# Optimization experiments

Hardware: AMD Instinct MI355X
Metric: run time of the kernel (lower is better)

Reference implementation:

```python
import jax, jax.numpy as jnp
import numpy as np

B, L, H, T, C = 4, 256, 768, 16, 6
SIM_THR = 0.0
EPS_LN = 1e-5


def layer_norm(x, g, b):
    m = x.mean(-1, keepdims=True)
    v = ((x - m) ** 2).mean(-1, keepdims=True)
    return (x - m) / jnp.sqrt(v + EPS_LN) * g + b


def setup_inputs() -> dict:
    key = jax.random.key(0)
    ks = jax.random.split(key, 20)
    s = 0.02
    embeddings = jax.random.normal(ks[0], (B, L, H), jnp.float32)
    masks = jnp.ones((B, L, L), jnp.float32)
    asp_st = jax.random.randint(ks[1], (B, T), 0, 12)
    asp_ed = asp_st + jax.random.randint(ks[2], (B, T), 0, 3)
    opi_st = jax.random.randint(ks[3], (B, T), 0, 12)
    opi_ed = opi_st + jax.random.randint(ks[4], (B, T), 0, 3)
    sent_id = jax.random.randint(ks[5], (B, T), 2, 5)
    return {
        "embeddings": embeddings, "masks": masks,
        "asp_st": asp_st, "asp_ed": asp_ed, "opi_st": opi_st, "opi_ed": opi_ed,
        "sent_id": sent_id,
        "edge_embed": jax.random.normal(ks[6], (2, H), jnp.float32) * s,
        "W_tp": jax.random.normal(ks[7], (2 * H + 3, H), jnp.float32) * s,
        "b_tp": jnp.zeros((H,), jnp.float32),
        "W_attn": jax.random.normal(ks[8], (3 * H, 1), jnp.float32) * s,
        "b_attn": jnp.zeros((1,), jnp.float32),
        "W_gat": jax.random.normal(ks[9], (2 * H, H), jnp.float32) * s,
        "b_gat": jnp.zeros((H,), jnp.float32),
        "gamma0": jnp.ones((H,), jnp.float32), "beta0": jnp.zeros((H,), jnp.float32),
        "W1": jax.random.normal(ks[10], (2 * H, L), jnp.float32) * s,
        "bl1": jnp.zeros((L,), jnp.float32),
        "gamma1": jnp.ones((L,), jnp.float32), "beta1": jnp.zeros((L,), jnp.float32),
        "Wc": jax.random.normal(ks[11], (L, C), jnp.float32) * s,
        "bc": jnp.zeros((C,), jnp.float32),
        "Wc1": jax.random.normal(ks[12], (L, 2), jnp.float32) * s,
        "bc1": jnp.zeros((2,), jnp.float32),
    }


def _triplet_enhance(emb_b, a_st, a_ed, o_st, o_ed, sid,
                     edge_embed, W_tp, b_tp, W_attn, b_attn, W_gat, b_gat):
    # emb_b: [L,H]; span ints: [T]
    pos = jnp.arange(L)
    am = (pos[None, :] >= a_st[:, None]) & (pos[None, :] <= a_ed[:, None])  # [T,L]
    om = (pos[None, :] >= o_st[:, None]) & (pos[None, :] <= o_ed[:, None])
    amf = am.astype(emb_b.dtype)
    omf = om.astype(emb_b.dtype)
    asp = (amf @ emb_b) / amf.sum(1, keepdims=True)  # [T,H] span-mean
    opi = (omf @ emb_b) / omf.sum(1, keepdims=True)
    sv = jax.nn.one_hot(sid - 2, 3, dtype=emb_b.dtype)  # [T,3]
    nf = jnp.concatenate([asp, opi, sv], -1) @ W_tp + b_tp  # [T,H]

    # cosine similarity between triplet nodes
    nrm = nf / jnp.maximum(jnp.linalg.norm(nf, axis=-1, keepdims=True), 1e-8)
    sim = nrm @ nrm.T
    eye = jnp.eye(T, dtype=bool)
    ok = (sim > SIM_THR) & ~eye
    m0 = ok & (a_st[:, None] == a_st[None, :]) & (a_ed[:, None] == a_ed[None, :])
    m1 = ok & (o_st[:, None] == o_st[None, :]) & (o_ed[:, None] == o_ed[None, :])
    # edge (i,j): src=i, tgt=j -> incoming mask indexed [tgt, src, etype]
    emask = jnp.stack([m0.T, m1.T], axis=-1)  # [T,T,2]

    E = edge_embed  # [2,H]
    cc = jnp.concatenate([
        jnp.broadcast_to(nf[:, None, None, :], (T, T, 2, H)),   # target feats
        jnp.broadcast_to(nf[None, :, None, :], (T, T, 2, H)),   # source feats
        jnp.broadcast_to(E[None, None, :, :], (T, T, 2, H)),
    ], -1)  # [T,T,2,3H]
    scores = (jax.nn.leaky_relu(cc, 0.2) @ W_attn)[..., 0] + b_attn[0]  # [T,T,2]
    neg = jnp.where(emask, scores, -1e9)
    attn = jax.nn.softmax(neg.reshape(T, -1), axis=-1).reshape(T, T, 2)
    msg = jnp.concatenate([
        jnp.broadcast_to(nf[:, None, :], (T, 2, H)),
        jnp.broadcast_to(E[None, :, :], (T, 2, H)),
    ], -1)  # [src, etype, 2H]
    agg = jnp.einsum('tse,sef->tf', attn, msg)
    upd = jax.nn.relu(agg @ W_gat + b_gat)
    has_in = emask.any(axis=(1, 2))
    new_nf = jnp.where(has_in[:, None], upd, nf)
    has_edges = emask.any().astype(emb_b.dtype)  # original skips scatter if no edges
    center = (a_st + o_st) // 2
    return emb_b.at[center].add(new_nf * has_edges)


def reference(embeddings, masks, asp_st, asp_ed, opi_st, opi_ed, sent_id,
              edge_embed, W_tp, b_tp, W_attn, b_attn, W_gat, b_gat,
              gamma0, beta0, W1, bl1, gamma1, beta1, Wc, bc, Wc1, bc1):
    emb1 = layer_norm(embeddings, gamma0, beta0)
    emb = jax.vmap(_triplet_enhance,
                   in_axes=(0, 0, 0, 0, 0, 0) + (None,) * 7)(
        emb1, asp_st, asp_ed, opi_st, opi_ed, sent_id,
        edge_embed, W_tp, b_tp, W_attn, b_attn, W_gat, b_gat)

    # cat([feat_exp, feat_expT]) @ W1  ==  emb@W1[:H] (rows) + emb@W1[H:] (cols)
    A = jnp.einsum('bih,hk->bik', emb, W1[:H])
    Bm = jnp.einsum('bjh,hk->bjk', emb, W1[H:])
    hidden = A[:, :, None, :] + Bm[:, None, :, :] + bl1  # [B,L,L,L]
    hidden = jax.nn.gelu(layer_norm(hidden, gamma1, beta1), approximate=False)
    logits = (hidden @ Wc + bc) * masks[..., None]    # [B,L,L,C]
    logits1 = (hidden @ Wc1 + bc1) * masks[..., None]  # [B,L,L,2]
    return jnp.concatenate([logits, logits1], -1)
```

## Files before the change

kernel.cpp:

```cpp
#include <hip/hip_runtime.h>

__device__ __forceinline__ unsigned short f2bf(float f) {
    union { float f; unsigned u; } v; v.f = f;
    unsigned u = v.u;
    unsigned r = (u + 0x7fffu + ((u >> 16) & 1u)) >> 16;
    return (unsigned short)r;
}
__device__ __forceinline__ float bfup(int x) {
    union { unsigned u; float f; } v; v.u = ((unsigned)(unsigned short)x) << 16; return v.f;
}

typedef __attribute__((ext_vector_type(8))) short short8;
typedef __attribute__((ext_vector_type(4))) float floatx4;

#define Bn 4
#define Ln 256
#define Hn 768
#define Tn 16

__global__ __launch_bounds__(256) void k_ln0(const float* __restrict__ x,
                                             const float* __restrict__ g,
                                             const float* __restrict__ be,
                                             float* __restrict__ out) {
    int row = blockIdx.x, tid = threadIdx.x;
    const float* xr = x + (size_t)row * Hn;
    float v0 = xr[tid], v1 = xr[tid + 256], v2 = xr[tid + 512];
    float s = v0 + v1 + v2;
    float q = v0 * v0 + v1 * v1 + v2 * v2;
    __shared__ float sm[4], qm[4];
    for (int o = 32; o > 0; o >>= 1) { s += __shfl_down(s, o); q += __shfl_down(q, o); }
    if ((tid & 63) == 0) { sm[tid >> 6] = s; qm[tid >> 6] = q; }
    __syncthreads();
    float S = sm[0] + sm[1] + sm[2] + sm[3];
    float Q = qm[0] + qm[1] + qm[2] + qm[3];
    float mean = S * (1.f / 768.f);
    float rstd = rsqrtf(Q * (1.f / 768.f) - mean * mean + 1e-5f);
    float* o0 = out + (size_t)row * Hn;
    o0[tid]       = (v0 - mean) * rstd * g[tid]       + be[tid];
    o0[tid + 256] = (v1 - mean) * rstd * g[tid + 256] + be[tid + 256];
    o0[tid + 512] = (v2 - mean) * rstd * g[tid + 512] + be[tid + 512];
}

__global__ __launch_bounds__(256) void k_spans(const float* __restrict__ emb,
                                               const int* __restrict__ ast_, const int* __restrict__ aed_,
                                               const int* __restrict__ ost_, const int* __restrict__ oed_,
                                               const int* __restrict__ sid_,
                                               float* __restrict__ xv,
                                               float* __restrict__ nf) {
    int n = blockIdx.x, b = n >> 4, tid = threadIdx.x;
    int ast = ast_[n], aed = aed_[n], ost = ost_[n], oed = oed_[n], sid = sid_[n];
    float ai = 1.f / (float)(aed - ast + 1);
    float oi = 1.f / (float)(oed - ost + 1);
    const float* eb = emb + (size_t)b * Ln * Hn;
    float* xr = xv + (size_t)n * 1568;
    for (int r = tid; r < 1568; r += 256) {
        float v;
        if (r < 768) {
            float s = 0.f;
            for (int l = ast; l <= aed; ++l) s += eb[l * Hn + r];
            v = s * ai;
        } else if (r < 1536) {
            int h = r - 768;
            float s = 0.f;
            for (int l = ost; l <= oed; ++l) s += eb[l * Hn + h];
            v = s * oi;
        } else if (r < 1539) {
            v = (sid - 2 == r - 1536) ? 1.f : 0.f;
        } else {
            v = 0.f;
        }
        xr[r] = v;
    }
    float* nr = nf + (size_t)n * Hn;
    nr[tid] = 0.f; nr[tid + 256] = 0.f; nr[tid + 512] = 0.f;
}

__global__ __launch_bounds__(256) void k_skinny(const float* __restrict__ A,
                                                const float* __restrict__ B,
                                                const float* __restrict__ bias,
                                                float* __restrict__ C,
                                                int Kpad, int Kb, int Kc) {
    __shared__ float At[32][33], Bt[32][33];
    int tid = threadIdx.x;
    int n0 = blockIdx.x * 32, m0 = blockIdx.y * 32, z = blockIdx.z;
    int kbeg = z * Kc;
    int kend = kbeg + Kc; if (kend > Kpad) kend = Kpad;
    int lr = tid >> 3, lc = (tid & 7) * 4;
    int tm = tid >> 3, tn4 = (tid & 7) * 4;
    float acc0 = 0.f, acc1 = 0.f, acc2 = 0.f, acc3 = 0.f;
    for (int k0 = kbeg; k0 < kend; k0 += 32) {
        float4 av = *(const float4*)(A + (size_t)(m0 + lr) * Kpad + k0 + lc);
        At[lr][lc] = av.x; At[lr][lc + 1] = av.y; At[lr][lc + 2] = av.z; At[lr][lc + 3] = av.w;
        int gk = k0 + lr;
        float4 bv = {0.f, 0.f, 0.f, 0.f};
        if (gk < Kb) bv = *(const float4*)(B + (size_t)gk * 768 + n0 + lc);
        Bt[lr][lc] = bv.x; Bt[lr][lc + 1] = bv.y; Bt[lr][lc + 2] = bv.z; Bt[lr][lc + 3] = bv.w;
        __syncthreads();
#pragma unroll
        for (int k = 0; k < 32; ++k) {
            float a = At[tm][k];
            acc0 = fmaf(a, Bt[k][tn4], acc0);
            acc1 = fmaf(a, Bt[k][tn4 + 1], acc1);
            acc2 = fmaf(a, Bt[k][tn4 + 2], acc2);
            acc3 = fmaf(a, Bt[k][tn4 + 3], acc3);
        }
        __syncthreads();
    }
    if (z == 0) {
        acc0 += bias[n0 + tn4];
        acc1 += bias[n0 + tn4 + 1];
        acc2 += bias[n0 + tn4 + 2];
        acc3 += bias[n0 + tn4 + 3];
    }
    float* dst = C + (size_t)(m0 + tm) * 768 + n0 + tn4;
    atomicAdd(&dst[0], acc0);
    atomicAdd(&dst[1], acc1);
    atomicAdd(&dst[2], acc2);
    atomicAdd(&dst[3], acc3);
}

__global__ __launch_bounds__(256) void k_graph(const float* __restrict__ nf,
                                               const int* __restrict__ ast_, const int* __restrict__ aed_,
                                               const int* __restrict__ ost_, const int* __restrict__ oed_,
                                               const float* __restrict__ E,
                                               const float* __restrict__ Wat,
                                               const float* __restrict__ bat,
                                               int* __restrict__ hasin, float* __restrict__ hasedge,
                                               float* __restrict__ agg, float* __restrict__ raw) {
    int b = blockIdx.x, tid = threadIdx.x;
    __shared__ float nfs[16][780];
    __shared__ float Es[2][768];
    __shared__ int ast[16], aed[16], ost[16], oed[16];
    __shared__ float red[256];
    __shared__ float nrm[16], p[16], q[16], rr[2];
    __shared__ float ws2[16][16];
    __shared__ float aes[16][2];
    __shared__ unsigned m0b[16], m1b[16];
    const float* nfb = nf + (size_t)b * 16 * Hn;
    for (int e = tid; e < 3072; e += 256) {
        int r = e / 192, c = (e - r * 192) * 4;
        float4 v = *(const float4*)(nfb + r * Hn + c);
        nfs[r][c] = v.x; nfs[r][c + 1] = v.y; nfs[r][c + 2] = v.z; nfs[r][c + 3] = v.w;
    }
    for (int e = tid; e < 1536; e += 256) ((float*)Es)[e] = E[e];
    if (tid < 16) {
        int n = b * 16 + tid;
        ast[tid] = ast_[n]; aed[tid] = aed_[n]; ost[tid] = ost_[n]; oed[tid] = oed_[n];
        m0b[tid] = 0u; m1b[tid] = 0u;
    }
    __syncthreads();
    int t = tid >> 4, lane = tid & 15;
    float ss = 0.f, pp = 0.f, qq = 0.f;
    for (int h = lane; h < 768; h += 16) {
        float v = nfs[t][h];
        ss = fmaf(v, v, ss);
        float lr = v > 0.f ? v : 0.2f * v;
        pp = fmaf(lr, Wat[h], pp);
        qq = fmaf(lr, Wat[768 + h], qq);
    }
    red[tid] = ss; __syncthreads();
    if (tid < 16) { float s = 0.f; for (int k2 = 0; k2 < 16; ++k2) s += red[tid * 16 + k2]; nrm[tid] = sqrtf(s); }
    __syncthreads();
    red[tid] = pp; __syncthreads();
    if (tid < 16) { float s = 0.f; for (int k2 = 0; k2 < 16; ++k2) s += red[tid * 16 + k2]; p[tid] = s; }
    __syncthreads();
    red[tid] = qq; __syncthreads();
    if (tid < 16) { float s = 0.f; for (int k2 = 0; k2 < 16; ++k2) s += red[tid * 16 + k2]; q[tid] = s; }
    __syncthreads();
    float rp = 0.f;
    if (tid < 32) {
        int e = tid >> 4;
        for (int h = lane; h < 768; h += 16) {
            float v = Es[e][h];
            float lr = v > 0.f ? v : 0.2f * v;
            rp = fmaf(lr, Wat[1536 + h], rp);
        }
    }
    red[tid] = rp; __syncthreads();
    if (tid < 2) { float s = 0.f; for (int k2 = 0; k2 < 16; ++k2) s += red[tid * 16 + k2]; rr[tid] = s; }
    __syncthreads();
    {
        int i = tid >> 4, j = tid & 15;
        const float4* ri = (const float4*)nfs[i];
        const float4* rj = (const float4*)nfs[j];
        float dot = 0.f;
#pragma unroll 4
        for (int h4 = 0; h4 < 192; ++h4) {
            float4 a = ri[h4], c = rj[h4];
            dot = fmaf(a.x, c.x, dot); dot = fmaf(a.y, c.y, dot);
            dot = fmaf(a.z, c.z, dot); dot = fmaf(a.w, c.w, dot);
        }
        float sim = dot / (fmaxf(nrm[i], 1e-8f) * fmaxf(nrm[j], 1e-8f));
        bool ok = (sim > 0.f) && (i != j);
        if (ok && ast[i] == ast[j] && aed[i] == aed[j]) atomicOr(&m0b[i], 1u << j);
        if (ok && ost[i] == ost[j] && oed[i] == oed[j]) atomicOr(&m1b[i], 1u << j);
    }
    __syncthreads();
    if (tid < 16) {
        int tt = tid;
        float battn = bat[0];
        float sc[32];
        float mx = -3.4e38f;
        bool hi = false;
#pragma unroll
        for (int s = 0; s < 16; ++s) {
            bool e0 = (m0b[s] >> tt) & 1u;
            bool e1 = (m1b[s] >> tt) & 1u;
            float base = p[tt] + q[s] + battn;
            float v0 = e0 ? (base + rr[0]) : -1e9f;
            float v1 = e1 ? (base + rr[1]) : -1e9f;
            sc[2 * s] = v0; sc[2 * s + 1] = v1;
            mx = fmaxf(mx, fmaxf(v0, v1));
            hi = hi || e0 || e1;
        }
        float sum = 0.f;
#pragma unroll
        for (int k2 = 0; k2 < 32; ++k2) { float e = expf(sc[k2] - mx); sc[k2] = e; sum += e; }
        float inv = 1.f / sum;
        float ae0 = 0.f, ae1 = 0.f;
#pragma unroll
        for (int s = 0; s < 16; ++s) {
            float w0 = sc[2 * s] * inv, w1 = sc[2 * s + 1] * inv;
            ws2[tt][s] = w0 + w1;
            ae0 += w0; ae1 += w1;
        }
        aes[tt][0] = ae0; aes[tt][1] = ae1;
        hasin[b * 16 + tt] = hi ? 1 : 0;
        red[tid] = hi ? 1.f : 0.f;
    }
    __syncthreads();
    if (tid == 0) {
        float he = 0.f;
        for (int k2 = 0; k2 < 16; ++k2) he = fmaxf(he, red[k2]);
        hasedge[b] = he;
    }
    for (int nn = 0; nn < 16; ++nn) {
        int n = b * 16 + nn;
        float ae0 = aes[nn][0], ae1 = aes[nn][1];
        float* ag = agg + (size_t)n * 1536;
        float* rw = raw + (size_t)n * Hn;
        for (int f = tid; f < 768; f += 256) {
            float s = 0.f;
#pragma unroll
            for (int s16 = 0; s16 < 16; ++s16) s = fmaf(ws2[nn][s16], nfs[s16][f], s);
            ag[f] = s;
            ag[768 + f] = ae0 * Es[0][f] + ae1 * Es[1][f];
            rw[f] = 0.f;
        }
    }
}

__global__ __launch_bounds__(256) void k_scatter(const float* __restrict__ raw,
                                                 const float* __restrict__ nf,
                                                 const int* __restrict__ hasin, const float* __restrict__ hasedge,
                                                 const int* __restrict__ ast_, const int* __restrict__ ost_,
                                                 float* __restrict__ emb) {
    int n = blockIdx.x, b = n >> 4, tid = threadIdx.x;
    if (hasedge[b] == 0.f) return;
    int center = (ast_[n] + ost_[n]) >> 1;
    float* dst = emb + (size_t)(b * Ln + center) * Hn;
    int hi = hasin[n];
    const float* src = hi ? (raw + (size_t)n * Hn) : (nf + (size_t)n * Hn);
    for (int h = tid; h < 768; h += 256) {
        float v = src[h];
        if (hi) v = fmaxf(v, 0.f);
        atomicAdd(&dst[h], v);
    }
}

__global__ __launch_bounds__(256) void k_w1t(const float* __restrict__ W1,
                                             unsigned short* __restrict__ w1t) {
    __shared__ float tile[32][33];
    int kt = blockIdx.x, nt = blockIdx.y, tid = threadIdx.x;
    int k0 = kt * 32, n0 = nt * 32;
    int rowoff = (n0 < 256) ? 0 : 768;
    int col0 = n0 & 255;
    int r = tid >> 3, c = (tid & 7) * 4;
    float4 v = *(const float4*)(W1 + (size_t)(rowoff + k0 + r) * 256 + col0 + c);
    tile[r][c] = v.x; tile[r][c + 1] = v.y; tile[r][c + 2] = v.z; tile[r][c + 3] = v.w;
    __syncthreads();
    ushort4 o;
    o.x = f2bf(tile[c][r]); o.y = f2bf(tile[c + 1][r]);
    o.z = f2bf(tile[c + 2][r]); o.w = f2bf(tile[c + 3][r]);
    *(ushort4*)(w1t + (size_t)(n0 + r) * 768 + k0 + c) = o;
}

__global__ __launch_bounds__(64) void k_gemm(const float* __restrict__ emb,
                                             const unsigned short* __restrict__ w1t,
                                             float* __restrict__ abm) {
    int wid = blockIdx.x;
    int m0 = (wid >> 4) * 32;
    int n0 = (wid & 15) * 32;
    int lane = threadIdx.x;
    int r = lane & 15, g = lane >> 4;
    const float* Af0 = emb + (size_t)(m0 + r) * 768 + g * 8;
    const float* Af1 = emb + (size_t)(m0 + 16 + r) * 768 + g * 8;
    const short8* Bp0 = (const short8*)(w1t + (size_t)(n0 + r) * 768 + g * 8);
    const short8* Bp1 = (const short8*)(w1t + (size_t)(n0 + 16 + r) * 768 + g * 8);
    floatx4 acc00 = {0.f, 0.f, 0.f, 0.f}, acc01 = {0.f, 0.f, 0.f, 0.f};
    floatx4 acc10 = {0.f, 0.f, 0.f, 0.f}, acc11 = {0.f, 0.f, 0.f, 0.f};
#pragma unroll 4
    for (int ks = 0; ks < 768; ks += 32) {
        float4 x0 = *(const float4*)(Af0 + ks);
        float4 x1 = *(const float4*)(Af0 + ks + 4);
        float4 y0 = *(const float4*)(Af1 + ks);
        float4 y1 = *(const float4*)(Af1 + ks + 4);
        short8 a0, a1;
        union { float f; unsigned u; } cv;
#define PK(dst, idx, val) { cv.f = (val); dst[idx] = (short)((cv.u + 0x8000u) >> 16); }
        PK(a0, 0, x0.x) PK(a0, 1, x0.y) PK(a0, 2, x0.z) PK(a0, 3, x0.w)
        PK(a0, 4, x1.x) PK(a0, 5, x1.y) PK(a0, 6, x1.z) PK(a0, 7, x1.w)
        PK(a1, 0, y0.x) PK(a1, 1, y0.y) PK(a1, 2, y0.z) PK(a1, 3, y0.w)
        PK(a1, 4, y1.x) PK(a1, 5, y1.y) PK(a1, 6, y1.z) PK(a1, 7, y1.w)
#undef PK
        short8 b0 = Bp0[ks >> 3];
        short8 b1 = Bp1[ks >> 3];
        acc00 = __builtin_amdgcn_mfma_f32_16x16x32_bf16(a0, b0, acc00, 0, 0, 0);
        acc01 = __builtin_amdgcn_mfma_f32_16x16x32_bf16(a0, b1, acc01, 0, 0, 0);
        acc10 = __builtin_amdgcn_mfma_f32_16x16x32_bf16(a1, b0, acc10, 0, 0, 0);
        acc11 = __builtin_amdgcn_mfma_f32_16x16x32_bf16(a1, b1, acc11, 0, 0, 0);
    }
#pragma unroll
    for (int t = 0; t < 4; ++t) {
        int row = g * 4 + t;
        abm[(size_t)(m0 + row) * 512 + n0 + r]           = acc00[t];
        abm[(size_t)(m0 + row) * 512 + n0 + 16 + r]      = acc01[t];
        abm[(size_t)(m0 + 16 + row) * 512 + n0 + r]      = acc10[t];
        abm[(size_t)(m0 + 16 + row) * 512 + n0 + 16 + r] = acc11[t];
    }
}

__global__ __launch_bounds__(256) void k_prep(const float* __restrict__ abm,
                                              const float* __restrict__ bl1,
                                              unsigned short* __restrict__ Abf,
                                              unsigned short* __restrict__ Bbf,
                                              float* __restrict__ sA, float* __restrict__ qA,
                                              float* __restrict__ sB, float* __restrict__ qB) {
    int rw = blockIdx.x, tid = threadIdx.x;
    float a = abm[(size_t)rw * 512 + tid];
    float bp = abm[(size_t)rw * 512 + 256 + tid] + bl1[tid];
    Abf[(size_t)rw * 256 + tid] = f2bf(a);
    Bbf[(size_t)rw * 256 + tid] = f2bf(bp);
    float v0 = a, v1 = a * a, v2 = bp, v3 = bp * bp;
    __shared__ float red[4][4];
    for (int o = 32; o > 0; o >>= 1) {
        v0 += __shfl_down(v0, o); v1 += __shfl_down(v1, o);
        v2 += __shfl_down(v2, o); v3 += __shfl_down(v3, o);
    }
    if ((tid & 63) == 0) {
        int w = tid >> 6;
        red[w][0] = v0; red[w][1] = v1; red[w][2] = v2; red[w][3] = v3;
    }
    __syncthreads();
    if (tid == 0) {
        sA[rw] = red[0][0] + red[1][0] + red[2][0] + red[3][0];
        qA[rw] = red[0][1] + red[1][1] + red[2][1] + red[3][1];
        sB[rw] = red[0][2] + red[1][2] + red[2][2] + red[3][2];
        qB[rw] = red[0][3] + red[1][3] + red[2][3] + red[3][3];
    }
}

__global__ __launch_bounds__(256) void k_dots(const float* __restrict__ abm,
                                              const float* __restrict__ bl1,
                                              float* __restrict__ D) {
    __shared__ float At[32][33], Bt[32][33];
    int tid = threadIdx.x;
    int j0 = blockIdx.x * 32, i0 = blockIdx.y * 32, b = blockIdx.z;
    int lr = tid >> 3, lc = (tid & 7) * 4;
    int ti = tid >> 3, tj4 = (tid & 7) * 4;
    float acc0 = 0.f, acc1 = 0.f, acc2 = 0.f, acc3 = 0.f;
    for (int k0 = 0; k0 < 256; k0 += 32) {
        float4 av = *(const float4*)(abm + (size_t)(b * 256 + i0 + lr) * 512 + k0 + lc);
        At[lr][lc] = av.x; At[lr][lc + 1] = av.y; At[lr][lc + 2] = av.z; At[lr][lc + 3] = av.w;
        float4 bv = *(const float4*)(abm + (size_t)(b * 256 + j0 + lr) * 512 + 256 + k0 + lc);
        float4 lv = *(const float4*)(bl1 + k0 + lc);
        Bt[lr][lc] = bv.x + lv.x; Bt[lr][lc + 1] = bv.y + lv.y;
        Bt[lr][lc + 2] = bv.z + lv.z; Bt[lr][lc + 3] = bv.w + lv.w;
        __syncthreads();
#pragma unroll
        for (int k = 0; k < 32; ++k) {
            float a = At[ti][k];
            acc0 = fmaf(a, Bt[tj4][k], acc0);
            acc1 = fmaf(a, Bt[tj4 + 1][k], acc1);
            acc2 = fmaf(a, Bt[tj4 + 2][k], acc2);
            acc3 = fmaf(a, Bt[tj4 + 3][k], acc3);
        }
        __syncthreads();
    }
    float* dst = D + ((size_t)b * 256 + i0 + ti) * 256 + j0 + tj4;
    dst[0] = acc0; dst[1] = acc1; dst[2] = acc2; dst[3] = acc3;
}

__global__ __launch_bounds__(256) void k_hidden2(const unsigned short* __restrict__ Abf,
                                                 const unsigned short* __restrict__ Bbf,
                                                 const float* __restrict__ sA, const float* __restrict__ qA,
                                                 const float* __restrict__ sB, const float* __restrict__ qB,
                                                 const float* __restrict__ D,
                                                 const float* __restrict__ masks,
                                                 const float* __restrict__ g1, const float* __restrict__ b1,
                                                 const float* __restrict__ Wc, const float* __restrict__ bc,
                                                 const float* __restrict__ Wc1, const float* __restrict__ bc1,
                                                 float* __restrict__ out) {
    __shared__ unsigned short As[16][272];
    __shared__ unsigned short Bs[16][272];
    __shared__ unsigned short gsh[256], bsh[256];
    __shared__ short8 Wf[8][64];
    __shared__ float Ds[16][16];
    __shared__ float ms[16][16];
    __shared__ float sAs[16], qAs[16], sBs[16], qBs[16];
    int tid = threadIdx.x;
    int jt = blockIdx.x, it = blockIdx.y, b = blockIdx.z;
    int rowA = b * 256 + it * 16;
    int rowB = b * 256 + jt * 16;
#pragma unroll
    for (int u = 0; u < 2; ++u) {
        int e = tid + u * 256;
        int r = e >> 5, ch = e & 31;
        *(short8*)&As[r][ch * 8] = *(const short8*)(Abf + (size_t)(rowA + r) * 256 + ch * 8);
        *(short8*)&Bs[r][ch * 8] = *(const short8*)(Bbf + (size_t)(rowB + r) * 256 + ch * 8);
    }
    gsh[tid] = f2bf(g1[tid]);
    bsh[tid] = f2bf(b1[tid]);
#pragma unroll
    for (int u = 0; u < 2; ++u) {
        int e = tid + u * 256;
        int s = e >> 6, l = e & 63;
        int qq2 = l >> 4, nn2 = l & 15;
        short8 wv;
#pragma unroll
        for (int t = 0; t < 8; ++t) {
            int k = s * 32 + qq2 * 8 + t;
            float v = (nn2 < 6) ? Wc[k * 6 + nn2] : ((nn2 < 8) ? Wc1[k * 2 + (nn2 - 6)] : 0.f);
            wv[t] = (short)f2bf(v);
        }
        Wf[s][l] = wv;
    }
    {
        int di = tid >> 4, dj = tid & 15;
        size_t gi = ((size_t)(b * 256 + it * 16 + di)) * 256 + jt * 16 + dj;
        Ds[di][dj] = D[gi];
        ms[di][dj] = masks[gi];
    }
    if (tid < 16) {
        sAs[tid] = sA[rowA + tid]; qAs[tid] = qA[rowA + tid];
        sBs[tid] = sB[rowB + tid]; qBs[tid] = qB[rowB + tid];
    }
    __syncthreads();

    int lane = tid & 63, w = tid >> 6;
    int m = lane & 15, q = lane >> 4;
    int iA = w * 4 + (m & 3);
    int n = m;
    float bcs_l = (n < 6) ? bc[n] : ((n < 8) ? bc1[n - 6] : 0.f);
    const float inv256 = 1.f / 256.f;
    const float K1 = -1.5957691216f, K2 = -0.0713548163f;

    for (int p = 0; p < 4; ++p) {
        int jB = p * 4 + (m >> 2);
        float mu = (sAs[iA] + sBs[jB]) * inv256;
        float E2 = (qAs[iA] + 2.f * Ds[iA][jB] + qBs[jB]) * inv256;
        float r_ = rsqrtf(E2 - mu * mu + 1e-5f);
        float c_ = -mu * r_;
        floatx4 acc = {0.f, 0.f, 0.f, 0.f};
#pragma unroll
        for (int s = 0; s < 8; ++s) {
            int ko = s * 32 + q * 8;
            short8 a8 = *(const short8*)&As[iA][ko];
            short8 b8 = *(const short8*)&Bs[jB][ko];
            short8 g8 = *(const short8*)&gsh[ko];
            short8 v8 = *(const short8*)&bsh[ko];
            short8 yv;
#pragma unroll
            for (int t = 0; t < 8; ++t) {
                float h = bfup(a8[t]) + bfup(b8[t]);
                float x = fmaf(h, r_, c_);
                x = fmaf(x, bfup(g8[t]), bfup(v8[t]));
                float mm = fmaf(x * x, K2, K1);
                float e = __expf(x * mm);
                float y = x * __builtin_amdgcn_rcpf(1.f + e);
                union { float f; unsigned u; } cv; cv.f = y;
                yv[t] = (short)((cv.u + 0x8000u) >> 16);
            }
            acc = __builtin_amdgcn_mfma_f32_16x16x32_bf16(yv, Wf[s][lane], acc, 0, 0, 0);
        }
        if (n < 8) {
#pragma unroll
            for (int rg = 0; rg < 4; ++rg) {
                int mp = q * 4 + rg;
                int il = w * 4 + (mp & 3);
                int jl = p * 4 + (mp >> 2);
                float mk = ms[il][jl];
                size_t idx = (((size_t)(b * 256 + it * 16 + il)) * 256 + jt * 16 + jl) * 8 + n;
                out[idx] = (acc[rg] + bcs_l) * mk;
            }
        }
    }
}

extern "C" void kernel_launch(void* const* d_in, const int* in_sizes, int n_in,
                              void* d_out, int out_size, void* d_ws, size_t ws_size,
                              hipStream_t stream) {
    (void)in_sizes; (void)n_in; (void)out_size; (void)ws_size;
    const float* emb_in = (const float*)d_in[0];
    const float* masks  = (const float*)d_in[1];
    const int* ast = (const int*)d_in[2];
    const int* aed = (const int*)d_in[3];
    const int* ost = (const int*)d_in[4];
    const int* oed = (const int*)d_in[5];
    const int* sid = (const int*)d_in[6];
    const float* E    = (const float*)d_in[7];
    const float* Wtp  = (const float*)d_in[8];
    const float* btp  = (const float*)d_in[9];
    const float* Wat  = (const float*)d_in[10];
    const float* bat  = (const float*)d_in[11];
    const float* Wg   = (const float*)d_in[12];
    const float* bg   = (const float*)d_in[13];
    const float* g0   = (const float*)d_in[14];
    const float* b0   = (const float*)d_in[15];
    const float* W1   = (const float*)d_in[16];
    const float* bl1  = (const float*)d_in[17];
    const float* g1   = (const float*)d_in[18];
    const float* b1   = (const float*)d_in[19];
    const float* Wc   = (const float*)d_in[20];
    const float* bc   = (const float*)d_in[21];
    const float* Wc1  = (const float*)d_in[22];
    const float* bc1  = (const float*)d_in[23];
    float* outp = (float*)d_out;

    float* fw = (float*)d_ws;
    float* emb = fw;
    float* nf  = fw + 786432;
    int*   hasin = (int*)(fw + 835584);
    float* hasedge = fw + 835648;
    float* xv  = fw + 835712;
    float* agg = fw + 936064;
    float* raw = fw + 1034368;
    float* Dd  = fw + 835712;
    float* abm = fw + 1097856;
    float* sA  = fw + 1622144;
    float* qA  = fw + 1623168;
    float* sB  = fw + 1624192;
    float* qB  = fw + 1625216;
    unsigned short* Abf = (unsigned short*)(fw + 1626240);
    unsigned short* Bbf = (unsigned short*)(fw + 1757312);
    unsigned short* w1t = (unsigned short*)(fw + 1888384);

    dim3 gw(24, 16);
    k_w1t<<<gw, 256, 0, stream>>>(W1, w1t);
    k_ln0<<<1024, 256, 0, stream>>>(emb_in, g0, b0, emb);
    k_spans<<<64, 256, 0, stream>>>(emb, ast, aed, ost, oed, sid, xv, nf);
    dim3 gs1(24, 2, 7);
    k_skinny<<<gs1, 256, 0, stream>>>(xv, Wtp, btp, nf, 1568, 1539, 224);
    k_graph<<<4, 256, 0, stream>>>(nf, ast, aed, ost, oed, E, Wat, bat, hasin, hasedge, agg, raw);
    k_skinny<<<gs1, 256, 0, stream>>>(agg, Wg, bg, raw, 1536, 1536, 224);
    k_scatter<<<64, 256, 0, stream>>>(raw, nf, hasin, hasedge, ast, ost, emb);
    k_gemm<<<512, 64, 0, stream>>>(emb, w1t, abm);
    k_prep<<<1024, 256, 0, stream>>>(abm, bl1, Abf, Bbf, sA, qA, sB, qB);
    dim3 gd(8, 8, 4);
    k_dots<<<gd, 256, 0, stream>>>(abm, bl1, Dd);
    dim3 g6(16, 16, 4);
    k_hidden2<<<g6, 256, 0, stream>>>(Abf, Bbf, sA, qA, sB, qB, Dd, masks,
                                      g1, b1, Wc, bc, Wc1, bc1, outp);
}
```

Measured before the change: 265.7 us.

## Fuse bf16 prep, row stats and A·B dot products into hidden kernel

Removes the k_prep and k_dots kernels. The hidden kernel now converts the fp32 A/B rows to bf16 itself, computes per-row sums and sums of squares, and computes the 16x16 cross-dot tile with one wave using MFMA. LN0 and the W1 transpose are merged into a single launch, and the LDS pitch is changed. This cuts launches and intermediate global round trips, at the cost of redundant per-tile conversion and reductions. The dot products and stats are now computed from bf16-rounded values, which slightly changes numerics.

```diff
diff --git a/kernel.cpp b/kernel.cpp
--- a/kernel.cpp
+++ b/kernel.cpp
@@ -17,28 +17,49 @@
 #define Ln 256
 #define Hn 768
 #define Tn 16
-
-__global__ __launch_bounds__(256) void k_ln0(const float* __restrict__ x,
+#define PITCH 288
+
+__global__ __launch_bounds__(256) void k_pre(const float* __restrict__ x,
                                              const float* __restrict__ g,
                                              const float* __restrict__ be,
-                                             float* __restrict__ out) {
-    int row = blockIdx.x, tid = threadIdx.x;
-    const float* xr = x + (size_t)row * Hn;
-    float v0 = xr[tid], v1 = xr[tid + 256], v2 = xr[tid + 512];
-    float s = v0 + v1 + v2;
-    float q = v0 * v0 + v1 * v1 + v2 * v2;
-    __shared__ float sm[4], qm[4];
-    for (int o = 32; o > 0; o >>= 1) { s += __shfl_down(s, o); q += __shfl_down(q, o); }
-    if ((tid & 63) == 0) { sm[tid >> 6] = s; qm[tid >> 6] = q; }
-    __syncthreads();
-    float S = sm[0] + sm[1] + sm[2] + sm[3];
-    float Q = qm[0] + qm[1] + qm[2] + qm[3];
-    float mean = S * (1.f / 768.f);
-    float rstd = rsqrtf(Q * (1.f / 768.f) - mean * mean + 1e-5f);
-    float* o0 = out + (size_t)row * Hn;
-    o0[tid]       = (v0 - mean) * rstd * g[tid]       + be[tid];
-    o0[tid + 256] = (v1 - mean) * rstd * g[tid + 256] + be[tid + 256];
-    o0[tid + 512] = (v2 - mean) * rstd * g[tid + 512] + be[tid + 512];
+                                             float* __restrict__ out,
+                                             const float* __restrict__ W1,
+                                             unsigned short* __restrict__ w1t) {
+    int bid = blockIdx.x, tid = threadIdx.x;
+    if (bid < 1024) {
+        int row = bid;
+        const float* xr = x + (size_t)row * Hn;
+        float v0 = xr[tid], v1 = xr[tid + 256], v2 = xr[tid + 512];
+        float s = v0 + v1 + v2;
+        float q = v0 * v0 + v1 * v1 + v2 * v2;
+        __shared__ float sm[4], qm[4];
+        for (int o = 32; o > 0; o >>= 1) { s += __shfl_down(s, o); q += __shfl_down(q, o); }
+        if ((tid & 63) == 0) { sm[tid >> 6] = s; qm[tid >> 6] = q; }
+        __syncthreads();
+        float S = sm[0] + sm[1] + sm[2] + sm[3];
+        float Q = qm[0] + qm[1] + qm[2] + qm[3];
+        float mean = S * (1.f / 768.f);
+        float rstd = rsqrtf(Q * (1.f / 768.f) - mean * mean + 1e-5f);
+        float* o0 = out + (size_t)row * Hn;
+        o0[tid]       = (v0 - mean) * rstd * g[tid]       + be[tid];
+        o0[tid + 256] = (v1 - mean) * rstd * g[tid + 256] + be[tid + 256];
+        o0[tid + 512] = (v2 - mean) * rstd * g[tid + 512] + be[tid + 512];
+    } else {
+        __shared__ float tile[32][33];
+        int idx = bid - 1024;
+        int kt = idx % 24, nt = idx / 24;
+        int k0 = kt * 32, n0 = nt * 32;
+        int rowoff = (n0 < 256) ? 0 : 768;
+        int col0 = n0 & 255;
+        int r = tid >> 3, c = (tid & 7) * 4;
+        float4 v = *(const float4*)(W1 + (size_t)(rowoff + k0 + r) * 256 + col0 + c);
+        tile[r][c] = v.x; tile[r][c + 1] = v.y; tile[r][c + 2] = v.z; tile[r][c + 3] = v.w;
+        __syncthreads();
+        ushort4 o;
+        o.x = f2bf(tile[c][r]); o.y = f2bf(tile[c + 1][r]);
+        o.z = f2bf(tile[c + 2][r]); o.w = f2bf(tile[c + 3][r]);
+        *(ushort4*)(w1t + (size_t)(n0 + r) * 768 + k0 + c) = o;
+    }
 }
 
 __global__ __launch_bounds__(256) void k_spans(const float* __restrict__ emb,
@@ -266,23 +287,6 @@
         if (hi) v = fmaxf(v, 0.f);
         atomicAdd(&dst[h], v);
     }
-}
-
-__global__ __launch_bounds__(256) void k_w1t(const float* __restrict__ W1,
-                                             unsigned short* __restrict__ w1t) {
-    __shared__ float tile[32][33];
-    int kt = blockIdx.x, nt = blockIdx.y, tid = threadIdx.x;
-    int k0 = kt * 32, n0 = nt * 32;
-    int rowoff = (n0 < 256) ? 0 : 768;
-    int col0 = n0 & 255;
-    int r = tid >> 3, c = (tid & 7) * 4;
-    float4 v = *(const float4*)(W1 + (size_t)(rowoff + k0 + r) * 256 + col0 + c);
-    tile[r][c] = v.x; tile[r][c + 1] = v.y; tile[r][c + 2] = v.z; tile[r][c + 3] = v.w;
-    __syncthreads();
-    ushort4 o;
-    o.x = f2bf(tile[c][r]); o.y = f2bf(tile[c + 1][r]);
-    o.z = f2bf(tile[c + 2][r]); o.w = f2bf(tile[c + 3][r]);
-    *(ushort4*)(w1t + (size_t)(n0 + r) * 768 + k0 + c) = o;
 }
 
 __global__ __launch_bounds__(64) void k_gemm(const float* __restrict__ emb,
@@ -330,94 +334,56 @@
     }
 }
 
-__global__ __launch_bounds__(256) void k_prep(const float* __restrict__ abm,
-                                              const float* __restrict__ bl1,
-                                              unsigned short* __restrict__ Abf,
-                                              unsigned short* __restrict__ Bbf,
-                                              float* __restrict__ sA, float* __restrict__ qA,
-                                              float* __restrict__ sB, float* __restrict__ qB) {
-    int rw = blockIdx.x, tid = threadIdx.x;
-    float a = abm[(size_t)rw * 512 + tid];
-    float bp = abm[(size_t)rw * 512 + 256 + tid] + bl1[tid];
-    Abf[(size_t)rw * 256 + tid] = f2bf(a);
-    Bbf[(size_t)rw * 256 + tid] = f2bf(bp);
-    float v0 = a, v1 = a * a, v2 = bp, v3 = bp * bp;
-    __shared__ float red[4][4];
-    for (int o = 32; o > 0; o >>= 1) {
-        v0 += __shfl_down(v0, o); v1 += __shfl_down(v1, o);
-        v2 += __shfl_down(v2, o); v3 += __shfl_down(v3, o);
-    }
-    if ((tid & 63) == 0) {
-        int w = tid >> 6;
-        red[w][0] = v0; red[w][1] = v1; red[w][2] = v2; red[w][3] = v3;
-    }
-    __syncthreads();
-    if (tid == 0) {
-        sA[rw] = red[0][0] + red[1][0] + red[2][0] + red[3][0];
-        qA[rw] = red[0][1] + red[1][1] + red[2][1] + red[3][1];
-        sB[rw] = red[0][2] + red[1][2] + red[2][2] + red[3][2];
-        qB[rw] = red[0][3] + red[1][3] + red[2][3] + red[3][3];
-    }
-}
-
-__global__ __launch_bounds__(256) void k_dots(const float* __restrict__ abm,
-                                              const float* __restrict__ bl1,
-                                              float* __restrict__ D) {
-    __shared__ float At[32][33], Bt[32][33];
-    int tid = threadIdx.x;
-    int j0 = blockIdx.x * 32, i0 = blockIdx.y * 32, b = blockIdx.z;
-    int lr = tid >> 3, lc = (tid & 7) * 4;
-    int ti = tid >> 3, tj4 = (tid & 7) * 4;
-    float acc0 = 0.f, acc1 = 0.f, acc2 = 0.f, acc3 = 0.f;
-    for (int k0 = 0; k0 < 256; k0 += 32) {
-        float4 av = *(const float4*)(abm + (size_t)(b * 256 + i0 + lr) * 512 + k0 + lc);
-        At[lr][lc] = av.x; At[lr][lc + 1] = av.y; At[lr][lc + 2] = av.z; At[lr][lc + 3] = av.w;
-        float4 bv = *(const float4*)(abm + (size_t)(b * 256 + j0 + lr) * 512 + 256 + k0 + lc);
-        float4 lv = *(const float4*)(bl1 + k0 + lc);
-        Bt[lr][lc] = bv.x + lv.x; Bt[lr][lc + 1] = bv.y + lv.y;
-        Bt[lr][lc + 2] = bv.z + lv.z; Bt[lr][lc + 3] = bv.w + lv.w;
-        __syncthreads();
-#pragma unroll
-        for (int k = 0; k < 32; ++k) {
-            float a = At[ti][k];
-            acc0 = fmaf(a, Bt[tj4][k], acc0);
-            acc1 = fmaf(a, Bt[tj4 + 1][k], acc1);
-            acc2 = fmaf(a, Bt[tj4 + 2][k], acc2);
-            acc3 = fmaf(a, Bt[tj4 + 3][k], acc3);
-        }
-        __syncthreads();
-    }
-    float* dst = D + ((size_t)b * 256 + i0 + ti) * 256 + j0 + tj4;
-    dst[0] = acc0; dst[1] = acc1; dst[2] = acc2; dst[3] = acc3;
-}
-
-__global__ __launch_bounds__(256) void k_hidden2(const unsigned short* __restrict__ Abf,
-                                                 const unsigned short* __restrict__ Bbf,
-                                                 const float* __restrict__ sA, const float* __restrict__ qA,
-                                                 const float* __restrict__ sB, const float* __restrict__ qB,
-                                                 const float* __restrict__ D,
-                                                 const float* __restrict__ masks,
-                                                 const float* __restrict__ g1, const float* __restrict__ b1,
-                                                 const float* __restrict__ Wc, const float* __restrict__ bc,
-                                                 const float* __restrict__ Wc1, const float* __restrict__ bc1,
-                                                 float* __restrict__ out) {
-    __shared__ unsigned short As[16][272];
-    __shared__ unsigned short Bs[16][272];
+__global__ __launch_bounds__(256, 4) void k_hidden3(const float* __restrict__ abm,
+                                                    const float* __restrict__ bl1,
+                                                    const float* __restrict__ masks,
+                                                    const float* __restrict__ g1, const float* __restrict__ b1,
+                                                    const float* __restrict__ Wc, const float* __restrict__ bc,
+                                                    const float* __restrict__ Wc1, const float* __restrict__ bc1,
+                                                    float* __restrict__ out) {
+    __shared__ unsigned short As[16][PITCH];
+    __shared__ unsigned short Bs[16][PITCH];
     __shared__ unsigned short gsh[256], bsh[256];
     __shared__ short8 Wf[8][64];
     __shared__ float Ds[16][16];
     __shared__ float ms[16][16];
+    __shared__ float red2[16][16][4];
     __shared__ float sAs[16], qAs[16], sBs[16], qBs[16];
     int tid = threadIdx.x;
     int jt = blockIdx.x, it = blockIdx.y, b = blockIdx.z;
     int rowA = b * 256 + it * 16;
     int rowB = b * 256 + jt * 16;
-#pragma unroll
-    for (int u = 0; u < 2; ++u) {
-        int e = tid + u * 256;
-        int r = e >> 5, ch = e & 31;
-        *(short8*)&As[r][ch * 8] = *(const short8*)(Abf + (size_t)(rowA + r) * 256 + ch * 8);
-        *(short8*)&Bs[r][ch * 8] = *(const short8*)(Bbf + (size_t)(rowB + r) * 256 + ch * 8);
+    {
+        int r = tid >> 4, sg = tid & 15;
+        const float* Ar = abm + (size_t)(rowA + r) * 512 + sg * 16;
+        const float* Br = abm + (size_t)(rowB + r) * 512 + 256 + sg * 16;
+        const float* Lr = bl1 + sg * 16;
+        float sa = 0.f, qa = 0.f, sb = 0.f, qb = 0.f;
+        short8 va0, va1, vb0, vb1;
+#pragma unroll
+        for (int u = 0; u < 4; ++u) {
+            float4 av = *(const float4*)(Ar + u * 4);
+            float4 bv = *(const float4*)(Br + u * 4);
+            float4 lv = *(const float4*)(Lr + u * 4);
+            float aa[4] = {av.x, av.y, av.z, av.w};
+            float bb[4] = {bv.x + lv.x, bv.y + lv.y, bv.z + lv.z, bv.w + lv.w};
+#pragma unroll
+            for (int e = 0; e < 4; ++e) {
+                unsigned short ah = f2bf(aa[e]), bh = f2bf(bb[e]);
+                float af = bfup(ah), bf2 = bfup(bh);
+                sa += af; qa = fmaf(af, af, qa);
+                sb += bf2; qb = fmaf(bf2, bf2, qb);
+                int pos = u * 4 + e;
+                if (pos < 8) { va0[pos] = (short)ah; vb0[pos] = (short)bh; }
+                else         { va1[pos - 8] = (short)ah; vb1[pos - 8] = (short)bh; }
+            }
+        }
+        *(short8*)&As[r][sg * 16]     = va0;
+        *(short8*)&As[r][sg * 16 + 8] = va1;
+        *(short8*)&Bs[r][sg * 16]     = vb0;
+        *(short8*)&Bs[r][sg * 16 + 8] = vb1;
+        red2[r][sg][0] = sa; red2[r][sg][1] = qa;
+        red2[r][sg][2] = sb; red2[r][sg][3] = qb;
     }
     gsh[tid] = f2bf(g1[tid]);
     bsh[tid] = f2bf(b1[tid]);
@@ -437,13 +403,30 @@
     }
     {
         int di = tid >> 4, dj = tid & 15;
-        size_t gi = ((size_t)(b * 256 + it * 16 + di)) * 256 + jt * 16 + dj;
-        Ds[di][dj] = D[gi];
-        ms[di][dj] = masks[gi];
-    }
-    if (tid < 16) {
-        sAs[tid] = sA[rowA + tid]; qAs[tid] = qA[rowA + tid];
-        sBs[tid] = sB[rowB + tid]; qBs[tid] = qB[rowB + tid];
+        ms[di][dj] = masks[((size_t)(b * 256 + it * 16 + di)) * 256 + jt * 16 + dj];
+    }
+    __syncthreads();
+    if (tid < 64) {
+        int m = tid & 15, q = tid >> 4;
+        floatx4 acc = {0.f, 0.f, 0.f, 0.f};
+#pragma unroll
+        for (int s = 0; s < 8; ++s) {
+            short8 a8 = *(const short8*)&As[m][s * 32 + q * 8];
+            short8 b8 = *(const short8*)&Bs[m][s * 32 + q * 8];
+            acc = __builtin_amdgcn_mfma_f32_16x16x32_bf16(a8, b8, acc, 0, 0, 0);
+        }
+#pragma unroll
+        for (int rg = 0; rg < 4; ++rg) Ds[q * 4 + rg][m] = acc[rg];
+    } else if (tid < 128) {
+        int t2 = tid - 64;
+        int which = t2 >> 4, r = t2 & 15;
+        float s = 0.f;
+#pragma unroll
+        for (int k2 = 0; k2 < 16; ++k2) s += red2[r][k2][which];
+        if (which == 0) sAs[r] = s;
+        else if (which == 1) qAs[r] = s;
+        else if (which == 2) sBs[r] = s;
+        else qBs[r] = s;
     }
     __syncthreads();
 
@@ -535,19 +518,10 @@
     float* xv  = fw + 835712;
     float* agg = fw + 936064;
     float* raw = fw + 1034368;
-    float* Dd  = fw + 835712;
-    float* abm = fw + 1097856;
-    float* sA  = fw + 1622144;
-    float* qA  = fw + 1623168;
-    float* sB  = fw + 1624192;
-    float* qB  = fw + 1625216;
-    unsigned short* Abf = (unsigned short*)(fw + 1626240);
-    unsigned short* Bbf = (unsigned short*)(fw + 1757312);
-    unsigned short* w1t = (unsigned short*)(fw + 1888384);
-
-    dim3 gw(24, 16);
-    k_w1t<<<gw, 256, 0, stream>>>(W1, w1t);
-    k_ln0<<<1024, 256, 0, stream>>>(emb_in, g0, b0, emb);
+    float* abm = fw + 1083520;
+    unsigned short* w1t = (unsigned short*)(fw + 1607808);
+
+    k_pre<<<1408, 256, 0, stream>>>(emb_in, g0, b0, emb, W1, w1t);
     k_spans<<<64, 256, 0, stream>>>(emb, ast, aed, ost, oed, sid, xv, nf);
     dim3 gs1(24, 2, 7);
     k_skinny<<<gs1, 256, 0, stream>>>(xv, Wtp, btp, nf, 1568, 1539, 224);
@@ -555,10 +529,6 @@
     k_skinny<<<gs1, 256, 0, stream>>>(agg, Wg, bg, raw, 1536, 1536, 224);
     k_scatter<<<64, 256, 0, stream>>>(raw, nf, hasin, hasedge, ast, ost, emb);
     k_gemm<<<512, 64, 0, stream>>>(emb, w1t, abm);
-    k_prep<<<1024, 256, 0, stream>>>(abm, bl1, Abf, Bbf, sA, qA, sB, qB);
-    dim3 gd(8, 8, 4);
-    k_dots<<<gd, 256, 0, stream>>>(abm, bl1, Dd);
     dim3 g6(16, 16, 4);
-    k_hidden2<<<g6, 256, 0, stream>>>(Abf, Bbf, sA, qA, sB, qB, Dd, masks,
-                                      g1, b1, Wc, bc, Wc1, bc1, outp);
-}
+    k_hidden3<<<g6, 256, 0, stream>>>(abm, bl1, masks, g1, b1, Wc, bc, Wc1, bc1, outp);
+}
```

Measured after the change: 302.2 us. 13.7% more time.
